# Kernel optimization log

Hardware: AMD Instinct MI355X
Metric: run time of the kernel (lower is better)

The kernel has to match this reference:

```python
import jax, jax.numpy as jnp
import numpy as np

B, C, L = 2048, 9605, 8
ALPHA = 0.5        # self.alpha
ALPHA1 = 0.05      # margin
ALPHA2 = 2.0       # asymmetric scale when violated
ALPHA3 = 5.0       # logistic sharpness
ALPHA_OTHER = 0.3  # floor on top-k threshold
TOPK = 16          # x_sorted[15] -> 16th largest


def setup_inputs() -> dict:
    key = jax.random.key(0)
    k1, k2, k3, k4 = jax.random.split(key, 4)
    x = jax.random.normal(k1, (B, C), dtype=jnp.float32)
    # each class assigned to one of 5*L slots; slots < L are whitelist groups,
    # the rest are 'other' classes (like total_indices in the torch code)
    gid = jax.random.randint(k4, (C,), 0, 5 * L)
    gid = gid.at[:L].set(jnp.arange(L))  # guarantee every group is non-empty
    group_mask = gid[None, :] == jnp.arange(L)[:, None]  # [L, C] bool
    # sparse multi-label binarized targets (~14 positives/sample)
    y = (jax.random.uniform(k2, (B, C)) < 0.0015).astype(jnp.float32)
    y_neg = (jax.random.uniform(k3, (B, C)) < 0.0015).astype(jnp.float32)
    return {"x": x, "y": y, "y_neg": y_neg, "group_mask": group_mask}


def _rank_loss(x1, x2):
    # our_rank_loss: sigmoid(alpha3*(x2-x1+margin)), scaled by alpha2 when violated
    d = x2 - x1 + ALPHA1
    s = jax.nn.sigmoid(ALPHA3 * d)
    return jnp.where(d > 0, ALPHA2 * s, s)


def reference(x, y, y_neg, group_mask):
    xs = jax.nn.sigmoid(x)  # [B, C]
    # top_k_thres = max(16th-largest sigmoid score, alpha_other)
    thres = jnp.maximum(jax.lax.top_k(xs, TOPK)[0][:, TOPK - 1], ALPHA_OTHER)  # [B]
    maskf = group_mask.astype(xs.dtype)  # [L, C]
    neg_inf = jnp.array(-jnp.inf, xs.dtype)
    # per-sample max score inside each whitelist group: [B, L]
    group_max = jnp.max(jnp.where(group_mask[None, :, :], xs[:, None, :], neg_inf), axis=-1)
    # find_gt_whitelist: group is 'hit' if any positive target inside it
    gt = (y @ maskf.T) > 0        # [B, L]
    gt_neg = (y_neg @ maskf.T) > 0  # [B, L]
    has_gt = jnp.any(gt, axis=-1)    # [B]; False <=> sentinel len(all_labels)
    has_neg = jnp.any(gt_neg, axis=-1)
    # ---- case B: sample hits at least one whitelist group ----
    rl_correct = _rank_loss(group_max, thres[:, None])    # gt groups above thres
    rl_incorrect = _rank_loss(thres[:, None], group_max)  # non-gt groups below thres
    caseB = jnp.sum(jnp.where(gt, rl_correct, rl_incorrect), axis=-1)  # [B]
    # ---- case A: no whitelist group hit ----
    union = jnp.any(group_mask, axis=0)  # [C] union of all whitelist classes
    union_max = jnp.max(jnp.where(union[None, :], xs, neg_inf), axis=-1)  # [B]
    neg_max = jnp.max(jnp.where(gt_neg, group_max, neg_inf), axis=-1)
    neg_score = jnp.where(has_neg, neg_max, jnp.zeros((), xs.dtype))  # torch starts at 0
    caseA = (1.0 - ALPHA) * _rank_loss(thres, union_max) + ALPHA * _rank_loss(thres, neg_score)
    loss_rank_all = jnp.where(has_gt, caseB, caseA)  # [B]
    return jnp.mean(loss_rank_all)
```

## Files before the change

### kernel.cpp

```cpp
#include <hip/hip_runtime.h>
#include <math.h>

constexpr int B_ = 2048;
constexpr int C_ = 9605;
constexpr int L_ = 8;
constexpr int TOPK_ = 16;
constexpr int CAPQ_ = 512;
constexpr int CAPC_ = 512;
constexpr float T0_ = 2.0f;
constexpr int CPAD_ = 9728;
constexpr int CS_ = 9632;
constexpr int CHCAP_ = 64;

__device__ __forceinline__ float sigm(float v) { return 1.0f / (1.0f + expf(-v)); }

__device__ __forceinline__ float rank_loss(float x1, float x2) {
  float d = x2 - x1 + 0.05f;
  float s = 1.0f / (1.0f + expf(-5.0f * d));
  return (d > 0.0f) ? 2.0f * s : s;
}

__device__ __forceinline__ unsigned int fkey(float v) {
  unsigned int u = __float_as_uint(v);
  return u ^ ((u & 0x80000000u) ? 0xFFFFFFFFu : 0x80000000u);
}
__device__ __forceinline__ float fkeyinv(unsigned int k) {
  unsigned int u = (k & 0x80000000u) ? (k ^ 0x80000000u) : ~k;
  return __uint_as_float(u);
}


__global__ void setup_kernel(const int* __restrict__ mask,
                             unsigned char* __restrict__ code4,
                             unsigned int* __restrict__ gslotG,
                             unsigned int* __restrict__ gtG,
                             unsigned int* __restrict__ gtnG,
                             int* __restrict__ cntG) {
  const int tid = blockIdx.x * 256 + threadIdx.x;
  if (tid < CS_ + 3) {
    unsigned char cd = 0xFF;
    if (tid < C_) {
#pragma unroll
      for (int l = L_ - 1; l >= 0; --l)
        if (mask[l * C_ + tid] != 0) cd = (unsigned char)l;
    }
#pragma unroll
    for (int ld = 0; ld < 4; ++ld) {
      int p = tid - ld;
      if (p >= 0 && p < CS_) code4[ld * CS_ + p] = cd;
    }
  }
  for (int i = tid; i < B_ * 8; i += 9728) gslotG[i] = 0x80000000u;
  for (int i = tid; i < B_; i += 9728) { gtG[i] = 0u; gtnG[i] = 0u; cntG[i] = 0; }
}

__global__ void __launch_bounds__(256, 8) sweep_kernel(
    const float* __restrict__ x, const float* __restrict__ y,
    const float* __restrict__ yn, const unsigned char* __restrict__ code4,
    unsigned int* __restrict__ gslotG, unsigned int* __restrict__ gtG,
    unsigned int* __restrict__ gtnG, int* __restrict__ cntG,
    float* __restrict__ candG) {
  constexpr int NE = B_ * C_;
  constexpr int TT = 2048 * 256;
  constexpr int NSTEP = (NE / 4 + TT - 1) / TT;
  __shared__ unsigned int ls[16];
  __shared__ unsigned int lbits[2];
  __shared__ float lcand[2][CHCAP_];
  __shared__ int lcnt[2], lbase[2];
  const int t = threadIdx.x;

  for (int step = 0; step < NSTEP; ++step) {
    const int qbase = step * TT + (int)blockIdx.x * 256;
    const int e0 = (qbase + t) << 2;
    const int efirst = qbase << 2;
    const int rfirst = efirst / C_;
    const bool act = (e0 < NE);
    float4 X, Y, N;
    if (act) {
      X = *reinterpret_cast<const float4*>(x + e0);
      Y = *reinterpret_cast<const float4*>(y + e0);
      N = *reinterpret_cast<const float4*>(yn + e0);
    }
    if (t < 16) ls[t] = 0x80000000u;
    if (t < 2) { lbits[t] = 0u; lcnt[t] = 0; }
    __syncthreads();

    if (act) {
      int r0 = e0 / C_;
      int cc = e0 - r0 * C_;
      int rr = r0 - rfirst;
      const bool fast = (cc + 3 < C_);
      unsigned int cw = 0u;
      if (fast)
        cw = *reinterpret_cast<const unsigned int*>(
            code4 + (size_t)((cc & 3) * CS_ + (cc & ~3)));
      const float xv[4] = {X.x, X.y, X.z, X.w};
      const float yv[4] = {Y.x, Y.y, Y.z, Y.w};
      const float nv[4] = {N.x, N.y, N.z, N.w};
#pragma unroll
      for (int k = 0; k < 4; ++k) {
        unsigned int cd = fast ? ((cw >> (8 * k)) & 0xFFu)
                               : (unsigned int)code4[cc];
        float xk = xv[k];
        if (cd < 8u) {
          if (xk > 0.0f) {
            unsigned int key = __float_as_uint(xk) | 0x80000000u;
            int a = rr * 8 + (int)cd;
            if (key > ls[a]) atomicMax(&ls[a], key);
          }
          if (yv[k] > 0.0f) atomicOr(&lbits[rr], 1u << cd);
          if (nv[k] > 0.0f) atomicOr(&lbits[rr], 1u << (8 + cd));
        }
        if (xk > T0_) {
          int p = atomicAdd(&lcnt[rr], 1);
          if (p < CHCAP_) {
            lcand[rr][p] = xk;
          } else {
            int g = atomicAdd(&cntG[rfirst + rr], 1);
            if (g < CAPC_) candG[(size_t)(rfirst + rr) * CAPC_ + g] = xk;
          }
        }
        if (++cc == C_) { cc = 0; ++rr; }
      }
    }
    __syncthreads();

    if (t < 16) {
      unsigned int v = ls[t];
      int row = rfirst + (t >> 3);
      if (v != 0x80000000u && row < B_) atomicMax(&gslotG[row * 8 + (t & 7)], v);
    }
    if (t < 2) {
      int row = rfirst + t;
      unsigned int bb = lbits[t];
      if (row < B_ && bb != 0u) {
        unsigned int g8 = bb & 0xFFu, n8 = (bb >> 8) & 0xFFu;
        if (g8) atomicOr(&gtG[row], g8);
        if (n8) atomicOr(&gtnG[row], n8);
      }
      int n = lcnt[t]; if (n > CHCAP_) n = CHCAP_;
      lbase[t] = (n > 0 && row < B_) ? atomicAdd(&cntG[row], n) : 0;
    }
    __syncthreads();
#pragma unroll
    for (int li = 0; li < 2; ++li) {
      int n = lcnt[li]; if (n > CHCAP_) n = CHCAP_;
      if (t < n) {
        int pos = lbase[li] + t;
        if (pos < CAPC_) candG[(size_t)(rfirst + li) * CAPC_ + pos] = lcand[li][t];
      }
    }
    __syncthreads();
  }
}

__global__ void finish_kernel(
    const float* __restrict__ x, const unsigned int* __restrict__ gslotG,
    const unsigned int* __restrict__ gtG, const unsigned int* __restrict__ gtnG,
    const int* __restrict__ cntG, const float* __restrict__ candG,
    float* __restrict__ loss) {
  const int r = blockIdx.x;
  const int t = threadIdx.x;
  const int cnt = cntG[r];
  float x16;
  if (cnt >= TOPK_ && cnt <= CAPC_) {
    const float* cf = candG + (size_t)r * CAPC_;
    unsigned int ku[CAPC_ / 64];
#pragma unroll
    for (int k = 0; k < CAPC_ / 64; ++k) {
      int i = t + (k << 6);
      ku[k] = (i < cnt) ? fkey(cf[i]) : 0u;
    }
    unsigned int lo = 0u, hi = 0xFFFFFFFFu;
#pragma unroll 1
    for (int it = 0; it < 32 && lo < hi; ++it) {
      unsigned int mid = lo + ((hi - lo) >> 1) + 1u;
      int c16 = 0;
#pragma unroll
      for (int k = 0; k < CAPC_ / 64; ++k) c16 += (ku[k] >= mid) ? 1 : 0;
#pragma unroll
      for (int off = 32; off > 0; off >>= 1) c16 += __shfl_xor(c16, off, 64);
      if (c16 >= TOPK_) lo = mid; else hi = mid - 1u;
    }
    x16 = fkeyinv(lo);
  } else {
    const float* xr = x + (size_t)r * C_;
    unsigned int lo = 0u, hi = 0xFFFFFFFFu;
#pragma unroll 1
    for (int it = 0; it < 32 && lo < hi; ++it) {
      unsigned int mid = lo + ((hi - lo) >> 1) + 1u;
      int cl = 0;
      for (int c = t; c < C_; c += 64) cl += (fkey(xr[c]) >= mid) ? 1 : 0;
#pragma unroll
      for (int off = 32; off > 0; off >>= 1) cl += __shfl_xor(cl, off, 64);
      if (cl >= TOPK_) lo = mid; else hi = mid - 1u;
    }
    x16 = fkeyinv(lo);
  }
  if (t == 0) {
    float thres = fmaxf(sigm(x16), 0.3f);
    unsigned int gtb = gtG[r], gnb = gtnG[r];
    float caseB = 0.0f, unio = -INFINITY, negmax = -INFINITY;
#pragma unroll
    for (int l = 0; l < L_; ++l) {
      float gm = __uint_as_float(gslotG[r * 8 + l] ^ 0x80000000u);
      float g = sigm(gm);
      unio = fmaxf(unio, g);
      caseB += ((gtb >> l) & 1u) ? rank_loss(g, thres) : rank_loss(thres, g);
      if ((gnb >> l) & 1u) negmax = fmaxf(negmax, g);
    }
    float negscore = (gnb != 0u) ? negmax : 0.0f;
    float caseA = 0.5f * rank_loss(thres, unio) + 0.5f * rank_loss(thres, negscore);
    loss[r] = (gtb != 0u) ? caseB : caseA;
  }
}


__global__ void build_code_kernel(const int* __restrict__ mask,
                                  unsigned char* __restrict__ code) {
  int c = blockIdx.x * 256 + threadIdx.x;
  if (c >= CPAD_) return;
  unsigned char cd = 0xFF;
  if (c < C_) {
#pragma unroll
    for (int l = L_ - 1; l >= 0; --l)
      if (mask[l * C_ + c] != 0) cd = (unsigned char)l;
  }
  code[c] = cd;
}

__global__ void __launch_bounds__(512, 4) row_loss_kernel(
    const float* __restrict__ x, const float* __restrict__ y,
    const float* __restrict__ yn, const unsigned char* __restrict__ code,
    float* __restrict__ loss) {
  __shared__ unsigned int lds_code[2404];
  __shared__ float4 cand4[CAPQ_];
  __shared__ unsigned int gslot[L_];
  __shared__ int cand_cnt;
  __shared__ unsigned int gt_bits, gtn_bits;
  __shared__ float s_x16;
  __shared__ int s_flag, s_red;

  const int t = threadIdx.x;
  const int b = blockIdx.x;
  const int lead = (4 - ((b * C_) & 3)) & 3;
  const int n4 = (C_ - lead) >> 2;

  const float* xb = x + (size_t)(b * C_ + lead);
  const float* yb = y + (size_t)(b * C_ + lead);
  const float* nb = yn + (size_t)(b * C_ + lead);

  if (t < L_) gslot[t] = 0x80000000u;
  if (t == 0) { cand_cnt = 0; gt_bits = 0u; gtn_bits = 0u; s_flag = 0; }

  const unsigned int* cdw = (const unsigned int*)code;
  if (lead == 0) {
    for (int j = t; j < n4; j += 512) lds_code[j] = cdw[j];
  } else {
    const int sh = lead << 3;
    for (int j = t; j < n4; j += 512) {
      unsigned int d0 = cdw[j], d1 = cdw[j + 1];
      lds_code[j] = (d0 >> sh) | (d1 << (32 - sh));
    }
  }
  __syncthreads();

  float4 XA, YA, NA, XB, YB, NB;

  auto ISSUE = [&](int j, float4& X, float4& Y, float4& N) {
    int js = (j < n4) ? j : 0;
    unsigned int vo = (unsigned int)js << 4;
    asm volatile("global_load_dwordx4 %0, %1, %2" : "=v"(X) : "v"(vo), "s"(xb));
    asm volatile("global_load_dwordx4 %0, %1, %2" : "=v"(Y) : "v"(vo), "s"(yb));
    asm volatile("global_load_dwordx4 %0, %1, %2" : "=v"(N) : "v"(vo), "s"(nb));
  };

  auto PROC = [&](const float4& X, const float4& Y, const float4& N, int j) {
    if (j >= n4) return;
    unsigned int cw = lds_code[j];
    float mx = fmaxf(fmaxf(X.x, X.y), fmaxf(X.z, X.w));
    if (mx > T0_) {
      int p = atomicAdd(&cand_cnt, 1);
      if (p < CAPQ_) cand4[p] = X;
    }
    {
      unsigned int cd, k;
      cd = cw & 0xFFu;
      if (cd < 8u && X.x > 0.0f) { k = __float_as_uint(X.x) | 0x80000000u; if (k > gslot[cd]) atomicMax(&gslot[cd], k); }
      cd = (cw >> 8) & 0xFFu;
      if (cd < 8u && X.y > 0.0f) { k = __float_as_uint(X.y) | 0x80000000u; if (k > gslot[cd]) atomicMax(&gslot[cd], k); }
      cd = (cw >> 16) & 0xFFu;
      if (cd < 8u && X.z > 0.0f) { k = __float_as_uint(X.z) | 0x80000000u; if (k > gslot[cd]) atomicMax(&gslot[cd], k); }
      cd = cw >> 24;
      if (cd < 8u && X.w > 0.0f) { k = __float_as_uint(X.w) | 0x80000000u; if (k > gslot[cd]) atomicMax(&gslot[cd], k); }
    }
    float sy = Y.x + Y.y + Y.z + Y.w + N.x + N.y + N.z + N.w;
    if (sy > 0.0f) {
      unsigned int d;
      d = cw & 0xFFu;
      if (d < 8u) { if (Y.x > 0.0f && !((gt_bits >> d) & 1u)) atomicOr(&gt_bits, 1u << d); if (N.x > 0.0f && !((gtn_bits >> d) & 1u)) atomicOr(&gtn_bits, 1u << d); }
      d = (cw >> 8) & 0xFFu;
      if (d < 8u) { if (Y.y > 0.0f && !((gt_bits >> d) & 1u)) atomicOr(&gt_bits, 1u << d); if (N.y > 0.0f && !((gtn_bits >> d) & 1u)) atomicOr(&gtn_bits, 1u << d); }
      d = (cw >> 16) & 0xFFu;
      if (d < 8u) { if (Y.z > 0.0f && !((gt_bits >> d) & 1u)) atomicOr(&gt_bits, 1u << d); if (N.z > 0.0f && !((gtn_bits >> d) & 1u)) atomicOr(&gtn_bits, 1u << d); }
      d = cw >> 24;
      if (d < 8u) { if (Y.w > 0.0f && !((gt_bits >> d) & 1u)) atomicOr(&gt_bits, 1u << d); if (N.w > 0.0f && !((gtn_bits >> d) & 1u)) atomicOr(&gtn_bits, 1u << d); }
    }
  };

  ISSUE(t, XA, YA, NA);
  ISSUE(t + 512, XB, YB, NB);

  asm volatile("s_waitcnt vmcnt(3)" ::: "memory");
  __builtin_amdgcn_sched_barrier(0);
  PROC(XA, YA, NA, t);
  ISSUE(t + 1024, XA, YA, NA);

  asm volatile("s_waitcnt vmcnt(3)" ::: "memory");
  __builtin_amdgcn_sched_barrier(0);
  PROC(XB, YB, NB, t + 512);
  ISSUE(t + 1536, XB, YB, NB);

  asm volatile("s_waitcnt vmcnt(3)" ::: "memory");
  __builtin_amdgcn_sched_barrier(0);
  PROC(XA, YA, NA, t + 1024);
  ISSUE(t + 2048, XA, YA, NA);

  asm volatile("s_waitcnt vmcnt(3)" ::: "memory");
  __builtin_amdgcn_sched_barrier(0);
  PROC(XB, YB, NB, t + 1536);

  asm volatile("s_waitcnt vmcnt(0)" ::: "memory");
  __builtin_amdgcn_sched_barrier(0);
  PROC(XA, YA, NA, t + 2048);

  if (t < 4) {
    auto sc = [&](int c) {
      float xv = x[(size_t)b * C_ + c], yv = y[(size_t)b * C_ + c],
            nv = yn[(size_t)b * C_ + c];
      unsigned int cd = code[c];
      if (cd < 8u) {
        if (xv > 0.0f) atomicMax(&gslot[cd], __float_as_uint(xv) | 0x80000000u);
        if (yv > 0.0f) atomicOr(&gt_bits, 1u << cd);
        if (nv > 0.0f) atomicOr(&gtn_bits, 1u << cd);
      }
      if (xv > T0_) {
        int p = atomicAdd(&cand_cnt, 1);
        if (p < CAPQ_) cand4[p] = make_float4(xv, -INFINITY, -INFINITY, -INFINITY);
      }
    };
    if (t < lead) sc(t);
    int c2 = lead + (n4 << 2) + t;
    if (c2 < C_) sc(c2);
  }
  __syncthreads();

  const int qn = cand_cnt;
  const bool ok_path = (qn >= 4) && (qn <= CAPQ_);
  if (ok_path && t < 64) {
    const float* cf = reinterpret_cast<const float*>(cand4);
    const int nvv = qn << 2;
    unsigned int ku[32];
#pragma unroll
    for (int k = 0; k < 32; ++k) {
      int i = t + (k << 6);
      ku[k] = (i < nvv) ? fkey(cf[i]) : 0u;
    }
    unsigned int lo = 0u, hi = 0xFFFFFFFFu;
#pragma unroll 1
    for (int it = 0; it < 32 && lo < hi; ++it) {
      unsigned int mid = lo + ((hi - lo) >> 1) + 1u;
      int c16 = 0;
#pragma unroll
      for (int k = 0; k < 32; ++k) c16 += (ku[k] >= mid) ? 1 : 0;
#pragma unroll
      for (int off = 32; off > 0; off >>= 1) c16 += __shfl_xor(c16, off, 64);
      if (c16 >= TOPK_) lo = mid; else hi = mid - 1u;
    }
    if (t == 0) {
      float v = fkeyinv(lo);
      s_x16 = v;
      s_flag = (v > T0_) ? 1 : 0;
    }
  }
  __syncthreads();
  if (!(ok_path && s_flag != 0)) {
    const float* xr = x + (size_t)b * C_;
    unsigned int lo = 0u, hi = 0xFFFFFFFFu;
    for (int it = 0; it < 32; ++it) {
      if (lo >= hi) break;
      unsigned int mid = lo + ((hi - lo) >> 1) + 1u;
      if (t == 0) s_red = 0;
      __syncthreads();
      int cl = 0;
      for (int c = t; c < C_; c += 512) cl += (fkey(xr[c]) >= mid) ? 1 : 0;
      atomicAdd(&s_red, cl);
      __syncthreads();
      int total = s_red;
      __syncthreads();
      if (total >= TOPK_) lo = mid; else hi = mid - 1u;
    }
    if (t == 0) s_x16 = fkeyinv(lo);
  }
  __syncthreads();

  if (t == 0) {
    float thres = fmaxf(sigm(s_x16), 0.3f);
    unsigned int gtb = gt_bits, gnb = gtn_bits;
    float caseB = 0.0f, unio = -INFINITY, negmax = -INFINITY;
#pragma unroll
    for (int l = 0; l < L_; ++l) {
      float gm = __uint_as_float(gslot[l] ^ 0x80000000u);
      float g = sigm(gm);
      unio = fmaxf(unio, g);
      caseB += ((gtb >> l) & 1u) ? rank_loss(g, thres) : rank_loss(thres, g);
      if ((gnb >> l) & 1u) negmax = fmaxf(negmax, g);
    }
    float negscore = (gnb != 0u) ? negmax : 0.0f;
    float caseA = 0.5f * rank_loss(thres, unio) + 0.5f * rank_loss(thres, negscore);
    loss[b] = (gtb != 0u) ? caseB : caseA;
  }
}

__global__ void mean_kernel(const float* __restrict__ loss, float* __restrict__ out) {
  const int t = threadIdx.x;
  float s = 0.0f;
  for (int i = t; i < B_; i += 256) s += loss[i];
#pragma unroll
  for (int off = 32; off > 0; off >>= 1) s += __shfl_xor(s, off, 64);
  __shared__ float part[4];
  if ((t & 63) == 0) part[t >> 6] = s;
  __syncthreads();
  if (t == 0) out[0] = (part[0] + part[1] + part[2] + part[3]) * (1.0f / (float)B_);
}

extern "C" void kernel_launch(void* const* d_in, const int* in_sizes, int n_in,
                              void* d_out, int out_size, void* d_ws, size_t ws_size,
                              hipStream_t stream) {
  const float* x = (const float*)d_in[0];
  const float* y = (const float*)d_in[1];
  const float* yn = (const float*)d_in[2];
  const int* mask = (const int*)d_in[3];

  constexpr size_t OFF_LOSS = 0;
  constexpr size_t OFF_CODE4 = 8192;
  constexpr size_t OFF_GSLOT = OFF_CODE4 + 4 * CS_;
  constexpr size_t OFF_GT = OFF_GSLOT + B_ * 8 * 4;
  constexpr size_t OFF_GTN = OFF_GT + B_ * 4;
  constexpr size_t OFF_CNT = OFF_GTN + B_ * 4;
  constexpr size_t OFF_CAND = OFF_CNT + B_ * 4;
  constexpr size_t WS_BIG = OFF_CAND + (size_t)B_ * CAPC_ * 4;

  float* loss = (float*)((char*)d_ws + OFF_LOSS);

  if (ws_size >= WS_BIG) {
    unsigned char* code4 = (unsigned char*)d_ws + OFF_CODE4;
    unsigned int* gslotG = (unsigned int*)((char*)d_ws + OFF_GSLOT);
    unsigned int* gtG = (unsigned int*)((char*)d_ws + OFF_GT);
    unsigned int* gtnG = (unsigned int*)((char*)d_ws + OFF_GTN);
    int* cntG = (int*)((char*)d_ws + OFF_CNT);
    float* candG = (float*)((char*)d_ws + OFF_CAND);

    hipLaunchKernelGGL(setup_kernel, dim3(38), dim3(256), 0, stream,
                       mask, code4, gslotG, gtG, gtnG, cntG);
    hipLaunchKernelGGL(sweep_kernel, dim3(2048), dim3(256), 0, stream,
                       x, y, yn, code4, gslotG, gtG, gtnG, cntG, candG);
    hipLaunchKernelGGL(finish_kernel, dim3(2048), dim3(64), 0, stream,
                       x, gslotG, gtG, gtnG, cntG, candG, loss);
  } else {
    unsigned char* code = (unsigned char*)d_ws + B_ * sizeof(float);
    hipLaunchKernelGGL(build_code_kernel, dim3((CPAD_ + 255) / 256), dim3(256), 0,
                       stream, mask, code);
    hipLaunchKernelGGL(row_loss_kernel, dim3(B_), dim3(512), 0, stream,
                       x, y, yn, code, loss);
  }
  hipLaunchKernelGGL(mean_kernel, dim3(1), dim3(256), 0, stream,
                     loss, (float*)d_out);
}
```

Before: 256.0 us.

## Split sweep into separate block groups for x, y and y_neg streams

The single sweep kernel is divided into three groups of 2048 blocks. One group processes x, handling group maxima and top-k candidates. The other two each scan one target array (y or y_neg) and OR in group-hit bits, and they skip the code lookup when a float4 has no positives. The aim is to spread the three streams over more concurrent blocks and lighten per-thread register and instruction load. The cost is extra block scheduling and more sync overhead in the lightweight target-scanning blocks.

```diff
diff --git a/kernel.cpp b/kernel.cpp
--- a/kernel.cpp
+++ b/kernel.cpp
@@ -54,7 +54,7 @@
   for (int i = tid; i < B_; i += 9728) { gtG[i] = 0u; gtnG[i] = 0u; cntG[i] = 0; }
 }
 
-__global__ void __launch_bounds__(256, 8) sweep_kernel(
+__global__ void __launch_bounds__(256, 8) sweep3_kernel(
     const float* __restrict__ x, const float* __restrict__ y,
     const float* __restrict__ yn, const unsigned char* __restrict__ code4,
     unsigned int* __restrict__ gslotG, unsigned int* __restrict__ gtG,
@@ -63,94 +63,120 @@
   constexpr int NE = B_ * C_;
   constexpr int TT = 2048 * 256;
   constexpr int NSTEP = (NE / 4 + TT - 1) / TT;
-  __shared__ unsigned int ls[16];
-  __shared__ unsigned int lbits[2];
-  __shared__ float lcand[2][CHCAP_];
-  __shared__ int lcnt[2], lbase[2];
   const int t = threadIdx.x;
-
-  for (int step = 0; step < NSTEP; ++step) {
-    const int qbase = step * TT + (int)blockIdx.x * 256;
-    const int e0 = (qbase + t) << 2;
-    const int efirst = qbase << 2;
-    const int rfirst = efirst / C_;
-    const bool act = (e0 < NE);
-    float4 X, Y, N;
-    if (act) {
-      X = *reinterpret_cast<const float4*>(x + e0);
-      Y = *reinterpret_cast<const float4*>(y + e0);
-      N = *reinterpret_cast<const float4*>(yn + e0);
-    }
-    if (t < 16) ls[t] = 0x80000000u;
-    if (t < 2) { lbits[t] = 0u; lcnt[t] = 0; }
-    __syncthreads();
-
-    if (act) {
-      int r0 = e0 / C_;
-      int cc = e0 - r0 * C_;
-      int rr = r0 - rfirst;
-      const bool fast = (cc + 3 < C_);
-      unsigned int cw = 0u;
-      if (fast)
-        cw = *reinterpret_cast<const unsigned int*>(
-            code4 + (size_t)((cc & 3) * CS_ + (cc & ~3)));
-      const float xv[4] = {X.x, X.y, X.z, X.w};
-      const float yv[4] = {Y.x, Y.y, Y.z, Y.w};
-      const float nv[4] = {N.x, N.y, N.z, N.w};
-#pragma unroll
-      for (int k = 0; k < 4; ++k) {
-        unsigned int cd = fast ? ((cw >> (8 * k)) & 0xFFu)
-                               : (unsigned int)code4[cc];
-        float xk = xv[k];
-        if (cd < 8u) {
-          if (xk > 0.0f) {
+  const int g = (int)blockIdx.x >> 11;
+  const int vb = (int)blockIdx.x & 2047;
+
+  if (g == 0) {
+    __shared__ unsigned int ls[16];
+    __shared__ float lcand[2][CHCAP_];
+    __shared__ int lcnt[2], lbase[2];
+
+    for (int step = 0; step < NSTEP; ++step) {
+      const int qbase = step * TT + vb * 256;
+      const int e0 = (qbase + t) << 2;
+      const int efirst = qbase << 2;
+      const int rfirst = efirst / C_;
+      const bool act = (e0 < NE);
+      float4 X;
+      if (act) X = *reinterpret_cast<const float4*>(x + e0);
+      if (t < 16) ls[t] = 0x80000000u;
+      if (t < 2) lcnt[t] = 0;
+      __syncthreads();
+
+      if (act) {
+        int r0 = e0 / C_;
+        int cc = e0 - r0 * C_;
+        int rr = r0 - rfirst;
+        const bool fast = (cc + 3 < C_);
+        unsigned int cw = 0u;
+        if (fast)
+          cw = *reinterpret_cast<const unsigned int*>(
+              code4 + (size_t)((cc & 3) * CS_ + (cc & ~3)));
+        const float xv[4] = {X.x, X.y, X.z, X.w};
+#pragma unroll
+        for (int k = 0; k < 4; ++k) {
+          unsigned int cd = fast ? ((cw >> (8 * k)) & 0xFFu)
+                                 : (unsigned int)code4[cc];
+          float xk = xv[k];
+          if (cd < 8u && xk > 0.0f) {
             unsigned int key = __float_as_uint(xk) | 0x80000000u;
             int a = rr * 8 + (int)cd;
             if (key > ls[a]) atomicMax(&ls[a], key);
           }
-          if (yv[k] > 0.0f) atomicOr(&lbits[rr], 1u << cd);
-          if (nv[k] > 0.0f) atomicOr(&lbits[rr], 1u << (8 + cd));
+          if (xk > T0_) {
+            int p = atomicAdd(&lcnt[rr], 1);
+            if (p < CHCAP_) {
+              lcand[rr][p] = xk;
+            } else {
+              int gi = atomicAdd(&cntG[rfirst + rr], 1);
+              if (gi < CAPC_) candG[(size_t)(rfirst + rr) * CAPC_ + gi] = xk;
+            }
+          }
+          if (++cc == C_) { cc = 0; ++rr; }
         }
-        if (xk > T0_) {
-          int p = atomicAdd(&lcnt[rr], 1);
-          if (p < CHCAP_) {
-            lcand[rr][p] = xk;
-          } else {
-            int g = atomicAdd(&cntG[rfirst + rr], 1);
-            if (g < CAPC_) candG[(size_t)(rfirst + rr) * CAPC_ + g] = xk;
+      }
+      __syncthreads();
+
+      if (t < 16) {
+        unsigned int v = ls[t];
+        int row = rfirst + (t >> 3);
+        if (v != 0x80000000u && row < B_) atomicMax(&gslotG[row * 8 + (t & 7)], v);
+      }
+      if (t < 2) {
+        int row = rfirst + t;
+        int n = lcnt[t]; if (n > CHCAP_) n = CHCAP_;
+        lbase[t] = (n > 0 && row < B_) ? atomicAdd(&cntG[row], n) : 0;
+      }
+      __syncthreads();
+#pragma unroll
+      for (int li = 0; li < 2; ++li) {
+        int n = lcnt[li]; if (n > CHCAP_) n = CHCAP_;
+        if (t < n) {
+          int pos = lbase[li] + t;
+          if (pos < CAPC_) candG[(size_t)(rfirst + li) * CAPC_ + pos] = lcand[li][t];
+        }
+      }
+      __syncthreads();
+    }
+  } else {
+    const float* src = (g == 1) ? y : yn;
+    unsigned int* dst = (g == 1) ? gtG : gtnG;
+    __shared__ unsigned int lbits[2];
+
+    for (int step = 0; step < NSTEP; ++step) {
+      const int qbase = step * TT + vb * 256;
+      const int e0 = (qbase + t) << 2;
+      const int efirst = qbase << 2;
+      const int rfirst = efirst / C_;
+      const bool act = (e0 < NE);
+      float4 V;
+      if (act) V = *reinterpret_cast<const float4*>(src + e0);
+      if (t < 2) lbits[t] = 0u;
+      __syncthreads();
+
+      if (act && (V.x > 0.0f || V.y > 0.0f || V.z > 0.0f || V.w > 0.0f)) {
+        int r0 = e0 / C_;
+        int cc = e0 - r0 * C_;
+        int rr = r0 - rfirst;
+        const float vv[4] = {V.x, V.y, V.z, V.w};
+#pragma unroll
+        for (int k = 0; k < 4; ++k) {
+          if (vv[k] > 0.0f) {
+            unsigned int cd = code4[cc];
+            if (cd < 8u) atomicOr(&lbits[rr], 1u << cd);
           }
+          if (++cc == C_) { cc = 0; ++rr; }
         }
-        if (++cc == C_) { cc = 0; ++rr; }
-      }
-    }
-    __syncthreads();
-
-    if (t < 16) {
-      unsigned int v = ls[t];
-      int row = rfirst + (t >> 3);
-      if (v != 0x80000000u && row < B_) atomicMax(&gslotG[row * 8 + (t & 7)], v);
-    }
-    if (t < 2) {
-      int row = rfirst + t;
-      unsigned int bb = lbits[t];
-      if (row < B_ && bb != 0u) {
-        unsigned int g8 = bb & 0xFFu, n8 = (bb >> 8) & 0xFFu;
-        if (g8) atomicOr(&gtG[row], g8);
-        if (n8) atomicOr(&gtnG[row], n8);
-      }
-      int n = lcnt[t]; if (n > CHCAP_) n = CHCAP_;
-      lbase[t] = (n > 0 && row < B_) ? atomicAdd(&cntG[row], n) : 0;
-    }
-    __syncthreads();
-#pragma unroll
-    for (int li = 0; li < 2; ++li) {
-      int n = lcnt[li]; if (n > CHCAP_) n = CHCAP_;
-      if (t < n) {
-        int pos = lbase[li] + t;
-        if (pos < CAPC_) candG[(size_t)(rfirst + li) * CAPC_ + pos] = lcand[li][t];
-      }
-    }
-    __syncthreads();
+      }
+      __syncthreads();
+      if (t < 2) {
+        int row = rfirst + t;
+        unsigned int bb = lbits[t];
+        if (row < B_ && bb != 0u) atomicOr(&dst[row], bb);
+      }
+      __syncthreads();
+    }
   }
 }
 
@@ -463,7 +489,7 @@
 
     hipLaunchKernelGGL(setup_kernel, dim3(38), dim3(256), 0, stream,
                        mask, code4, gslotG, gtG, gtnG, cntG);
-    hipLaunchKernelGGL(sweep_kernel, dim3(2048), dim3(256), 0, stream,
+    hipLaunchKernelGGL(sweep3_kernel, dim3(3 * 2048), dim3(256), 0, stream,
                        x, y, yn, code4, gslotG, gtG, gtnG, cntG, candG);
     hipLaunchKernelGGL(finish_kernel, dim3(2048), dim3(64), 0, stream,
                        x, gslotG, gtG, gtnG, cntG, candG, loss);
```

New measurement: 251.6 us. No clear change (-1.7%).
